# Optimization experiments

Measured on AMD Instinct MI355X. Metric: run time of the kernel, lower is better.

## Reference

```python
import jax, jax.numpy as jnp
import numpy as np

B, D3, L, H, O, E, GH = 4096, 288, 32, 512, 96, 8, 128


def _init_linear(key, out_dim, in_dim):
    kw, kb = jax.random.split(key)
    bound = 1.0 / np.sqrt(in_dim)
    W = jax.random.uniform(kw, (out_dim, in_dim), jnp.float32, -bound, bound)
    b = jax.random.uniform(kb, (out_dim,), jnp.float32, -bound, bound)
    return W, b


def setup_inputs() -> dict:
    key = jax.random.key(0)
    ks = jax.random.split(key, 12)
    x = jax.random.normal(ks[0], (B, D3), jnp.float32)
    z = jax.random.normal(ks[1], (B, L), jnp.float32)
    # per-expert weights, stacked on leading expert axis [E, out, in]
    def expert_stack(k, out_dim, in_dim):
        Ws, bs = [], []
        for i in range(E):
            Wi, bi = _init_linear(jax.random.fold_in(k, i), out_dim, in_dim)
            Ws.append(Wi); bs.append(bi)
        return jnp.stack(Ws), jnp.stack(bs)
    W0, b0 = expert_stack(ks[2], H, D3 + L)
    W1, b1 = expert_stack(ks[3], H, H + L)
    W2, b2 = expert_stack(ks[4], H, H + L)
    W3, b3 = expert_stack(ks[5], O, H)
    gW1, gb1 = _init_linear(ks[6], GH, D3 + L)
    gW2, gb2 = _init_linear(ks[7], GH, GH)
    gW3, gb3 = _init_linear(ks[8], E, GH)
    return {"x": x, "z": z, "W0": W0, "b0": b0, "W1": W1, "b1": b1,
            "W2": W2, "b2": b2, "W3": W3, "b3": b3,
            "gW1": gW1, "gb1": gb1, "gW2": gW2, "gb2": gb2,
            "gW3": gW3, "gb3": gb3}


def _gating(x, z, gW1, gb1, gW2, gb2, gW3, gb3):
    h = jnp.concatenate([x, z], axis=1)
    h = jax.nn.elu(h @ gW1.T + gb1)
    h = jax.nn.elu(h @ gW2.T + gb2)
    return jax.nn.softmax(h @ gW3.T + gb3, axis=-1)  # [B, E]


def _blended_linear(g, W, b, h):
    # Original: materializes sum_e g[b,e] * W_e -> [B,out,in], then bmm.
    # Mathematically identical linear form: sum_e g[b,e] * (W_e h_b + b_e).
    return jnp.einsum('be,eoi,bi->bo', g, W, h) + g @ b


def reference(x, z, W0, b0, W1, b1, W2, b2, W3, b3,
              gW1, gb1, gW2, gb2, gW3, gb3):
    g = _gating(x, z, gW1, gb1, gW2, gb2, gW3, gb3)  # [B, E]
    # dropout p=0.0 (eval) -> identity
    h = jax.nn.elu(_blended_linear(g, W0, b0, jnp.concatenate([x, z], axis=1)))
    h = jax.nn.elu(_blended_linear(g, W1, b1, jnp.concatenate([h, z], axis=1)))
    h = jax.nn.elu(_blended_linear(g, W2, b2, jnp.concatenate([h, z], axis=1)))
    out = _blended_linear(g, W3, b3, h)
    return out  # [B, O]
```

## Files before the change

### kernel.cpp

```cpp
#include <hip/hip_runtime.h>
#include <hip/hip_fp16.h>

typedef _Float16 half8 __attribute__((ext_vector_type(8)));
typedef _Float16 half4 __attribute__((ext_vector_type(4)));
typedef float floatx4 __attribute__((ext_vector_type(4)));

__device__ __forceinline__ void async_ld16(const void* g, void* l) {
    __builtin_amdgcn_global_load_lds(
        (const __attribute__((address_space(1))) char*)g,
        (__attribute__((address_space(3))) char*)l, 16, 0, 0);
}

__device__ __forceinline__ float elu_f(float v) {
    return v > 0.f ? v : (__expf(v) - 1.f);
}

__device__ __forceinline__ half4 cvt4(const float* src, int j4) {
    float4 f = ((const float4*)src)[j4];
    half4 h; h.x = (_Float16)f.x; h.y = (_Float16)f.y;
    h.z = (_Float16)f.z; h.w = (_Float16)f.w; return h;
}

__launch_bounds__(256)
__global__ void convert_all(const float* __restrict__ x, const float* __restrict__ z,
                            const float* __restrict__ W0, const float* __restrict__ W1,
                            const float* __restrict__ W2, const float* __restrict__ W3,
                            const float* __restrict__ gW1, const float* __restrict__ gW2,
                            const float* __restrict__ gW3,
                            _Float16* __restrict__ X0,
                            _Float16* __restrict__ h0, _Float16* __restrict__ h1,
                            _Float16* __restrict__ h2,
                            _Float16* __restrict__ Wc0, _Float16* __restrict__ Wc1,
                            _Float16* __restrict__ Wc2, _Float16* __restrict__ Wc3,
                            _Float16* __restrict__ gW1c, _Float16* __restrict__ gW2c,
                            _Float16* __restrict__ gW3c)
{
    const int S0 = 294912;
    const int S1 = 32768;
    const int S2 = 327680;
    const int S3 = 589824;
    const int S4 = 589824;
    const int S5 = 98304;
    const int S6 = 196608;
    const int S7 = 10240;
    const int S8 = 4096;
    const int TOTAL = S0 + S1 + S2 + S3 + S4 + S5 + S6 + S7 + S8 + 256;
    const half4 hz = {};

    for (int i = blockIdx.x * blockDim.x + threadIdx.x; i < TOTAL;
         i += gridDim.x * blockDim.x) {
        int j = i;
        if (j < S0) {
            int r = j / 72, c = j - r * 72;
            *(half4*)(X0 + r * 320 + c * 4) = cvt4(x, j);
            continue;
        }
        j -= S0;
        if (j < S1) {
            int r = j / 8, c = j - r * 8;
            *(half4*)(X0 + r * 320 + 288 + c * 4) = cvt4(z, j);
            continue;
        }
        j -= S1;
        if (j < S2) { *(half4*)(Wc0 + j * 4) = cvt4(W0, j); continue; }
        j -= S2;
        if (j < S3) {
            int r = j / 144, c = j - r * 144;
            *(half4*)(Wc1 + r * 576 + c * 4) = (c < 136) ? cvt4(W1, r * 136 + c) : hz;
            continue;
        }
        j -= S3;
        if (j < S4) {
            int r = j / 144, c = j - r * 144;
            *(half4*)(Wc2 + r * 576 + c * 4) = (c < 136) ? cvt4(W2, r * 136 + c) : hz;
            continue;
        }
        j -= S4;
        if (j < S5) { *(half4*)(Wc3 + j * 4) = cvt4(W3, j); continue; }
        j -= S5;
        if (j < S6) {
            int buf = j >> 16;
            int r2 = j & 65535;
            int row = r2 >> 4, c = r2 & 15;
            _Float16* h = (buf == 0) ? h0 : ((buf == 1) ? h1 : h2);
            *(half4*)(h + row * 576 + 512 + c * 4) = (c < 8) ? cvt4(z, row * 8 + c) : hz;
            continue;
        }
        j -= S6;
        if (j < S7) { *(half4*)(gW1c + j * 4) = cvt4(gW1, j); continue; }
        j -= S7;
        if (j < S8) { *(half4*)(gW2c + j * 4) = cvt4(gW2, j); continue; }
        j -= S8;
        *(half4*)(gW3c + j * 4) = cvt4(gW3, j);
    }
}

__launch_bounds__(256)
__global__ void gating_fast(const _Float16* __restrict__ X0,
                            const _Float16* __restrict__ gW1c,
                            const _Float16* __restrict__ gW2c,
                            const _Float16* __restrict__ gW3c,
                            const float* __restrict__ gb1,
                            const float* __restrict__ gb2,
                            const float* __restrict__ gb3,
                            float* __restrict__ g)
{
    __shared__ _Float16 Tbuf[4 * 16 * 136];

    const int tid = threadIdx.x;
    const int l = tid & 63;
    const int w = tid >> 6;
    const int quad = l >> 4;
    const int mi = l & 15;
    const int kq = quad * 8;
    const int mrow = (blockIdx.x * 4 + w) * 16;

    _Float16* T = Tbuf + w * (16 * 136);
    const _Float16* arow = X0 + (size_t)(mrow + mi) * 320;

    floatx4 acc1[8] = {};
    half8 a_nxt = *(const half8*)(arow + kq);
#pragma unroll
    for (int kc = 0; kc < 10; kc++) {
        const int k0 = kc * 32;
        half8 a = a_nxt;
        if (kc < 9) a_nxt = *(const half8*)(arow + k0 + 32 + kq);
#pragma unroll
        for (int t = 0; t < 8; t++) {
            half8 b = *(const half8*)(gW1c + (size_t)(t * 16 + mi) * 320 + k0 + kq);
            acc1[t] = __builtin_amdgcn_mfma_f32_16x16x32_f16(a, b, acc1[t], 0, 0, 0);
        }
    }
#pragma unroll
    for (int t = 0; t < 8; t++) {
        const int n = t * 16 + mi;
        const float bn = gb1[n];
#pragma unroll
        for (int r = 0; r < 4; r++)
            T[(quad * 4 + r) * 136 + n] = (_Float16)elu_f(acc1[t][r] + bn);
    }

    floatx4 acc2[8] = {};
#pragma unroll
    for (int kc = 0; kc < 4; kc++) {
        const int k0 = kc * 32;
        half8 a = *(const half8*)(T + mi * 136 + k0 + kq);
#pragma unroll
        for (int t = 0; t < 8; t++) {
            half8 b = *(const half8*)(gW2c + (size_t)(t * 16 + mi) * 128 + k0 + kq);
            acc2[t] = __builtin_amdgcn_mfma_f32_16x16x32_f16(a, b, acc2[t], 0, 0, 0);
        }
    }
#pragma unroll
    for (int t = 0; t < 8; t++) {
        const int n = t * 16 + mi;
        const float bn = gb2[n];
#pragma unroll
        for (int r = 0; r < 4; r++)
            T[(quad * 4 + r) * 136 + n] = (_Float16)elu_f(acc2[t][r] + bn);
    }

    floatx4 acc3 = {};
#pragma unroll
    for (int kc = 0; kc < 4; kc++) {
        const int k0 = kc * 32;
        half8 a = *(const half8*)(T + mi * 136 + k0 + kq);
        half8 b = (mi < 8) ? *(const half8*)(gW3c + (size_t)mi * 128 + k0 + kq) : half8{};
        acc3 = __builtin_amdgcn_mfma_f32_16x16x32_f16(a, b, acc3, 0, 0, 0);
    }
    const float gb = gb3[mi & 7];
#pragma unroll
    for (int r = 0; r < 4; r++) {
        float logit = acc3[r] + gb;
        float mx = logit;
        mx = fmaxf(mx, __shfl_xor(mx, 1));
        mx = fmaxf(mx, __shfl_xor(mx, 2));
        mx = fmaxf(mx, __shfl_xor(mx, 4));
        float e = __expf(logit - mx);
        float s = e;
        s += __shfl_xor(s, 1);
        s += __shfl_xor(s, 2);
        s += __shfl_xor(s, 4);
        if (mi < 8)
            g[(size_t)(mrow + quad * 4 + r) * 8 + mi] = e / s;
    }
}

template <bool ELU_ACT, typename OUT_T>
__launch_bounds__(256, 4)
__global__ void blend64(const _Float16* __restrict__ A, int lda,
                        const _Float16* __restrict__ W, int ldw,
                        int Hdim, int K,
                        const float* __restrict__ g,
                        const float* __restrict__ bias,
                        OUT_T* __restrict__ out, int ldo)
{
    __shared__ __align__(16) char smem_raw[32768];
    _Float16* sA = (_Float16*)smem_raw;
    _Float16* sB = (_Float16*)(smem_raw + 16384);
    float* sredf = (float*)smem_raw;
    __shared__ float sg[128][9];
    __shared__ float sbias[8][16];

    const int tid = threadIdx.x;
    const int l = tid & 63;
    const int w = tid >> 6;
    const int wm = w >> 1, wn = w & 1;
    const int o0 = blockIdx.x * 16;
    const int m0 = blockIdx.y * 128;

    for (int t = tid; t < 128 * 8; t += 256)
        sg[t >> 3][t & 7] = g[(size_t)(m0 + (t >> 3)) * 8 + (t & 7)];
    for (int t = tid; t < 128; t += 256)
        sbias[t >> 4][t & 15] = bias[(t >> 4) * Hdim + o0 + (t & 15)];

    const int lr = l >> 3;
    const int lc = l & 7;
    const int swz = lc ^ lr;

    const _Float16* gAp = A + (size_t)(m0 + w * 64 + lr) * lda + swz * 8;
    _Float16* lAp = sA + w * 4096;
    const int wb = w - 2;
    const int eb = wb * 4;
    const _Float16* gBe = W + ((size_t)eb * Hdim + o0 + lr) * ldw + swz * 8;
    const _Float16* gBo = gBe + (size_t)8 * ldw;
    _Float16* lBp = sB + wb * 4096;

    const int mi = l & 15, quad = l >> 4;
    const int cswz = mi & 7;
    const int offh0 = ((quad ^ cswz) * 8);
    const int offh1 = (((quad + 4) ^ cswz) * 8);
    const _Float16* rAb = sA + (wm * 64 + mi) * 64;
    const _Float16* rBb = sB + (wn * 64 + mi) * 64;

    floatx4 acc[4][4] = {};

    for (int k0 = 0; k0 < K; k0 += 64) {
        __syncthreads();
        if (w < 2) {
            const _Float16* gp = gAp + k0;
            _Float16* lp = lAp;
#pragma unroll
            for (int c = 0; c < 8; c++) {
                async_ld16(gp, lp);
                gp += (size_t)8 * lda;
                lp += 512;
            }
        } else {
            const _Float16* ge = gBe + k0;
            const _Float16* go = gBo + k0;
            _Float16* lp = lBp;
#pragma unroll
            for (int c2 = 0; c2 < 4; c2++) {
                async_ld16(ge, lp); lp += 512;
                async_ld16(go, lp); lp += 512;
                ge += (size_t)Hdim * ldw;
                go += (size_t)Hdim * ldw;
            }
        }
        __syncthreads();
#pragma unroll
        for (int h = 0; h < 2; h++) {
            const int off = h ? offh1 : offh0;
            half8 af[4], bf[4];
#pragma unroll
            for (int i = 0; i < 4; i++) af[i] = *(const half8*)(rAb + i * 1024 + off);
#pragma unroll
            for (int j = 0; j < 4; j++) bf[j] = *(const half8*)(rBb + j * 1024 + off);
#pragma unroll
            for (int i = 0; i < 4; i++)
#pragma unroll
                for (int j = 0; j < 4; j++)
                    acc[i][j] = __builtin_amdgcn_mfma_f32_16x16x32_f16(af[i], bf[j], acc[i][j], 0, 0, 0);
        }
    }

    float p[4][4];
#pragma unroll
    for (int i = 0; i < 4; i++)
#pragma unroll
        for (int r = 0; r < 4; r++) {
            int mloc = wm * 64 + i * 16 + quad * 4 + r;
            float s = 0.f;
#pragma unroll
            for (int j = 0; j < 4; j++) {
                int e = wn * 4 + j;
                s += sg[mloc][e] * (acc[i][j][r] + sbias[e][mi]);
            }
            p[i][r] = s;
        }

    __syncthreads();
    if (wn == 0) {
#pragma unroll
        for (int i = 0; i < 4; i++)
#pragma unroll
            for (int r = 0; r < 4; r++)
                sredf[(wm * 64 + i * 16 + quad * 4 + r) * 17 + mi] = p[i][r];
    }
    __syncthreads();
    if (wn == 1) {
#pragma unroll
        for (int i = 0; i < 4; i++)
#pragma unroll
            for (int r = 0; r < 4; r++) {
                int mrel = i * 16 + quad * 4 + r;
                float v = p[i][r] + sredf[(wm * 64 + mrel) * 17 + mi];
                if (ELU_ACT) v = elu_f(v);
                out[(size_t)(m0 + wm * 64 + mrel) * ldo + o0 + mi] = (OUT_T)v;
            }
    }
}

extern "C" void kernel_launch(void* const* d_in, const int* in_sizes, int n_in,
                              void* d_out, int out_size, void* d_ws, size_t ws_size,
                              hipStream_t stream)
{
    (void)in_sizes; (void)n_in; (void)out_size; (void)ws_size;
    const float* x   = (const float*)d_in[0];
    const float* z   = (const float*)d_in[1];
    const float* W0  = (const float*)d_in[2];
    const float* b0  = (const float*)d_in[3];
    const float* W1  = (const float*)d_in[4];
    const float* b1  = (const float*)d_in[5];
    const float* W2  = (const float*)d_in[6];
    const float* b2  = (const float*)d_in[7];
    const float* W3  = (const float*)d_in[8];
    const float* b3  = (const float*)d_in[9];
    const float* gW1 = (const float*)d_in[10];
    const float* gb1 = (const float*)d_in[11];
    const float* gW2 = (const float*)d_in[12];
    const float* gb2 = (const float*)d_in[13];
    const float* gW3 = (const float*)d_in[14];
    const float* gb3 = (const float*)d_in[15];

    char* p = (char*)d_ws;
    auto alloc = [&](size_t n) { char* r = p; p += (n + 255) & ~(size_t)255; return r; };
    _Float16* X0   = (_Float16*)alloc((size_t)4096 * 320 * 2);
    _Float16* h0   = (_Float16*)alloc((size_t)4096 * 576 * 2);
    _Float16* h1   = (_Float16*)alloc((size_t)4096 * 576 * 2);
    _Float16* h2   = (_Float16*)alloc((size_t)4096 * 576 * 2);
    _Float16* Wc0  = (_Float16*)alloc((size_t)8 * 512 * 320 * 2);
    _Float16* Wc1  = (_Float16*)alloc((size_t)8 * 512 * 576 * 2);
    _Float16* Wc2  = (_Float16*)alloc((size_t)8 * 512 * 576 * 2);
    _Float16* Wc3  = (_Float16*)alloc((size_t)8 * 96 * 512 * 2);
    _Float16* gW1c = (_Float16*)alloc((size_t)128 * 320 * 2);
    _Float16* gW2c = (_Float16*)alloc((size_t)128 * 128 * 2);
    _Float16* gW3c = (_Float16*)alloc((size_t)8 * 128 * 2);
    float*    g    = (float*)alloc((size_t)4096 * 8 * 4);

    convert_all<<<1024, 256, 0, stream>>>(x, z, W0, W1, W2, W3, gW1, gW2, gW3,
                                          X0, h0, h1, h2, Wc0, Wc1, Wc2, Wc3,
                                          gW1c, gW2c, gW3c);

    gating_fast<<<64, 256, 0, stream>>>(X0, gW1c, gW2c, gW3c, gb1, gb2, gb3, g);

    blend64<true, _Float16><<<dim3(32, 32), 256, 0, stream>>>(X0, 320, Wc0, 320, 512, 320, g, b0, h0, 576);
    blend64<true, _Float16><<<dim3(32, 32), 256, 0, stream>>>(h0, 576, Wc1, 576, 512, 576, g, b1, h1, 576);
    blend64<true, _Float16><<<dim3(32, 32), 256, 0, stream>>>(h1, 576, Wc2, 576, 512, 576, g, b2, h2, 576);
    blend64<false, float><<<dim3(6, 32), 256, 0, stream>>>(h2, 576, Wc3, 512, 96, 512, g, b3, (float*)d_out, 96);
}
```

Before: 192.8 us.

## Enlarge blend tiles to 256x32 with 1024-thread blocks and double-buffered LDS

Replaces the 128-row, 16-column blended-GEMM block with a 256-row, 32-column block of 16 waves. It double-buffers the async global-to-LDS loads so the next K-slice loads while MFMAs run on the current one. The larger tile raises operand reuse and removes one barrier per iteration. In exchange it uses 128KB of LDS per block, which limits occupancy to one block per CU and sharply cuts the grid size (the final layer gets only 48 blocks). It also adds a multi-step cross-wave reduction.

```diff
diff --git a/kernel.cpp b/kernel.cpp
--- a/kernel.cpp
+++ b/kernel.cpp
@@ -187,86 +187,77 @@
 }
 
 template <bool ELU_ACT, typename OUT_T>
-__launch_bounds__(256, 4)
-__global__ void blend64(const _Float16* __restrict__ A, int lda,
-                        const _Float16* __restrict__ W, int ldw,
-                        int Hdim, int K,
-                        const float* __restrict__ g,
-                        const float* __restrict__ bias,
-                        OUT_T* __restrict__ out, int ldo)
+__launch_bounds__(1024, 4)
+__global__ void blend_big(const _Float16* __restrict__ A, int lda,
+                          const _Float16* __restrict__ W, int ldw,
+                          int Hdim, int K,
+                          const float* __restrict__ g,
+                          const float* __restrict__ bias,
+                          OUT_T* __restrict__ out, int ldo)
 {
-    __shared__ __align__(16) char smem_raw[32768];
-    _Float16* sA = (_Float16*)smem_raw;
-    _Float16* sB = (_Float16*)(smem_raw + 16384);
-    float* sredf = (float*)smem_raw;
-    __shared__ float sg[128][9];
-    __shared__ float sbias[8][16];
+    __shared__ __align__(16) char smem[131072];
+    __shared__ float sg[256][9];
+    __shared__ float sbias[8][32];
+    _Float16* const sbase = (_Float16*)smem;
+    float* const sred = (float*)smem;
 
     const int tid = threadIdx.x;
     const int l = tid & 63;
     const int w = tid >> 6;
-    const int wm = w >> 1, wn = w & 1;
-    const int o0 = blockIdx.x * 16;
-    const int m0 = blockIdx.y * 128;
-
-    for (int t = tid; t < 128 * 8; t += 256)
+    const int wm = w >> 2, wn = w & 3;
+    const int o0 = blockIdx.x * 32;
+    const int m0 = blockIdx.y * 256;
+
+    for (int t = tid; t < 2048; t += 1024)
         sg[t >> 3][t & 7] = g[(size_t)(m0 + (t >> 3)) * 8 + (t & 7)];
-    for (int t = tid; t < 128; t += 256)
-        sbias[t >> 4][t & 15] = bias[(t >> 4) * Hdim + o0 + (t & 15)];
+    if (tid < 256)
+        sbias[tid >> 5][tid & 31] = bias[(tid >> 5) * Hdim + o0 + (tid & 31)];
 
     const int lr = l >> 3;
     const int lc = l & 7;
     const int swz = lc ^ lr;
-
-    const _Float16* gAp = A + (size_t)(m0 + w * 64 + lr) * lda + swz * 8;
-    _Float16* lAp = sA + w * 4096;
-    const int wb = w - 2;
-    const int eb = wb * 4;
-    const _Float16* gBe = W + ((size_t)eb * Hdim + o0 + lr) * ldw + swz * 8;
-    const _Float16* gBo = gBe + (size_t)8 * ldw;
-    _Float16* lBp = sB + wb * 4096;
+    const int sw = w & 7;
+    const bool isB = (w >= 8);
+    const _Float16* gS = isB
+        ? W + ((size_t)(sw * Hdim + o0 + lr)) * ldw + swz * 8
+        : A + ((size_t)(m0 + sw * 32 + lr)) * lda + swz * 8;
+    const int ldS = isB ? ldw : lda;
+    _Float16* const lS = sbase + (isB ? 16384 : 0) + sw * 2048;
 
     const int mi = l & 15, quad = l >> 4;
     const int cswz = mi & 7;
-    const int offh0 = ((quad ^ cswz) * 8);
-    const int offh1 = (((quad + 4) ^ cswz) * 8);
-    const _Float16* rAb = sA + (wm * 64 + mi) * 64;
-    const _Float16* rBb = sB + (wn * 64 + mi) * 64;
+    const _Float16* const rA0 = sbase + (wm * 64 + mi) * 64;
+    const _Float16* const rB0 = sbase + 16384 + (wn * 64 + mi) * 64;
 
     floatx4 acc[4][4] = {};
-
-    for (int k0 = 0; k0 < K; k0 += 64) {
+    const int NIT = K >> 6;
+
+    {
+        const _Float16* gp = gS;
+#pragma unroll
+        for (int c = 0; c < 4; c++)
+            async_ld16(gp + (size_t)c * 8 * ldS, lS + c * 512);
+    }
+
+    for (int it = 0; it < NIT; it++) {
         __syncthreads();
-        if (w < 2) {
-            const _Float16* gp = gAp + k0;
-            _Float16* lp = lAp;
-#pragma unroll
-            for (int c = 0; c < 8; c++) {
-                async_ld16(gp, lp);
-                gp += (size_t)8 * lda;
-                lp += 512;
-            }
-        } else {
-            const _Float16* ge = gBe + k0;
-            const _Float16* go = gBo + k0;
-            _Float16* lp = lBp;
-#pragma unroll
-            for (int c2 = 0; c2 < 4; c2++) {
-                async_ld16(ge, lp); lp += 512;
-                async_ld16(go, lp); lp += 512;
-                ge += (size_t)Hdim * ldw;
-                go += (size_t)Hdim * ldw;
-            }
-        }
-        __syncthreads();
+        if (it + 1 < NIT) {
+            const _Float16* gp = gS + (it + 1) * 64;
+            _Float16* lp = lS + ((it + 1) & 1) * 32768;
+#pragma unroll
+            for (int c = 0; c < 4; c++)
+                async_ld16(gp + (size_t)c * 8 * ldS, lp + c * 512);
+        }
+        const _Float16* pA = rA0 + (it & 1) * 32768;
+        const _Float16* pB = rB0 + (it & 1) * 32768;
 #pragma unroll
         for (int h = 0; h < 2; h++) {
-            const int off = h ? offh1 : offh0;
+            const int off = ((h * 4 + quad) ^ cswz) * 8;
             half8 af[4], bf[4];
 #pragma unroll
-            for (int i = 0; i < 4; i++) af[i] = *(const half8*)(rAb + i * 1024 + off);
-#pragma unroll
-            for (int j = 0; j < 4; j++) bf[j] = *(const half8*)(rBb + j * 1024 + off);
+            for (int i = 0; i < 4; i++) af[i] = *(const half8*)(pA + i * 1024 + off);
+#pragma unroll
+            for (int j = 0; j < 4; j++) bf[j] = *(const half8*)(pB + j * 1024 + off);
 #pragma unroll
             for (int i = 0; i < 4; i++)
 #pragma unroll
@@ -275,39 +266,72 @@
         }
     }
 
-    float p[4][4];
+    float p[4][2][4];
 #pragma unroll
     for (int i = 0; i < 4; i++)
 #pragma unroll
         for (int r = 0; r < 4; r++) {
-            int mloc = wm * 64 + i * 16 + quad * 4 + r;
-            float s = 0.f;
-#pragma unroll
-            for (int j = 0; j < 4; j++) {
-                int e = wn * 4 + j;
-                s += sg[mloc][e] * (acc[i][j][r] + sbias[e][mi]);
+            const int mrel = wm * 64 + i * 16 + quad * 4 + r;
+            const int e0 = wn * 2;
+#pragma unroll
+            for (int hf = 0; hf < 2; hf++) {
+                p[i][hf][r] = sg[mrel][e0]     * (acc[i][hf][r]     + sbias[e0][hf * 16 + mi])
+                            + sg[mrel][e0 + 1] * (acc[i][hf + 2][r] + sbias[e0 + 1][hf * 16 + mi]);
             }
-            p[i][r] = s;
-        }
-
+        }
+
+    __syncthreads();
+    if (wn & 1) {
+        float* dst = sred + (size_t)(wn >> 1) * 256 * 33;
+#pragma unroll
+        for (int i = 0; i < 4; i++)
+#pragma unroll
+            for (int r = 0; r < 4; r++) {
+                const int mrel = wm * 64 + i * 16 + quad * 4 + r;
+#pragma unroll
+                for (int hf = 0; hf < 2; hf++)
+                    dst[mrel * 33 + hf * 16 + mi] = p[i][hf][r];
+            }
+    }
+    __syncthreads();
+    if (!(wn & 1)) {
+        const float* srcp = sred + (size_t)(wn >> 1) * 256 * 33;
+#pragma unroll
+        for (int i = 0; i < 4; i++)
+#pragma unroll
+            for (int r = 0; r < 4; r++) {
+                const int mrel = wm * 64 + i * 16 + quad * 4 + r;
+#pragma unroll
+                for (int hf = 0; hf < 2; hf++)
+                    p[i][hf][r] += srcp[mrel * 33 + hf * 16 + mi];
+            }
+        if (wn == 2) {
+            float* dst = sred + 256 * 33;
+#pragma unroll
+            for (int i = 0; i < 4; i++)
+#pragma unroll
+                for (int r = 0; r < 4; r++) {
+                    const int mrel = wm * 64 + i * 16 + quad * 4 + r;
+#pragma unroll
+                    for (int hf = 0; hf < 2; hf++)
+                        dst[mrel * 33 + hf * 16 + mi] = p[i][hf][r];
+                }
+        }
+    }
     __syncthreads();
     if (wn == 0) {
+        const float* srcp = sred + 256 * 33;
 #pragma unroll
         for (int i = 0; i < 4; i++)
 #pragma unroll
-            for (int r = 0; r < 4; r++)
-                sredf[(wm * 64 + i * 16 + quad * 4 + r) * 17 + mi] = p[i][r];
-    }
-    __syncthreads();
-    if (wn == 1) {
-#pragma unroll
-        for (int i = 0; i < 4; i++)
-#pragma unroll
             for (int r = 0; r < 4; r++) {
-                int mrel = i * 16 + quad * 4 + r;
-                float v = p[i][r] + sredf[(wm * 64 + mrel) * 17 + mi];
-                if (ELU_ACT) v = elu_f(v);
-                out[(size_t)(m0 + wm * 64 + mrel) * ldo + o0 + mi] = (OUT_T)v;
+                const int mrel = wm * 64 + i * 16 + quad * 4 + r;
+#pragma unroll
+                for (int hf = 0; hf < 2; hf++) {
+                    float v = p[i][hf][r] + srcp[mrel * 33 + hf * 16 + mi];
+                    if (ELU_ACT) v = elu_f(v);
+                    out[(size_t)(m0 + mrel) * ldo + o0 + hf * 16 + mi] = (OUT_T)v;
+                }
             }
     }
 }
@@ -355,8 +379,8 @@
 
     gating_fast<<<64, 256, 0, stream>>>(X0, gW1c, gW2c, gW3c, gb1, gb2, gb3, g);
 
-    blend64<true, _Float16><<<dim3(32, 32), 256, 0, stream>>>(X0, 320, Wc0, 320, 512, 320, g, b0, h0, 576);
-    blend64<true, _Float16><<<dim3(32, 32), 256, 0, stream>>>(h0, 576, Wc1, 576, 512, 576, g, b1, h1, 576);
-    blend64<true, _Float16><<<dim3(32, 32), 256, 0, stream>>>(h1, 576, Wc2, 576, 512, 576, g, b2, h2, 576);
-    blend64<false, float><<<dim3(6, 32), 256, 0, stream>>>(h2, 576, Wc3, 512, 96, 512, g, b3, (float*)d_out, 96);
-}
+    blend_big<true, _Float16><<<dim3(16, 16), 1024, 0, stream>>>(X0, 320, Wc0, 320, 512, 320, g, b0, h0, 576);
+    blend_big<true, _Float16><<<dim3(16, 16), 1024, 0, stream>>>(h0, 576, Wc1, 576, 512, 576, g, b1, h1, 576);
+    blend_big<true, _Float16><<<dim3(16, 16), 1024, 0, stream>>>(h1, 576, Wc2, 576, 512, 576, g, b2, h2, 576);
+    blend_big<false, float><<<dim3(3, 16), 1024, 0, stream>>>(h2, 576, Wc3, 512, 96, 512, g, b3, (float*)d_out, 96);
+}
```

Measured after the change: 203.3 us. 5.5% more time.
